# Kernel optimization log

Hardware: AMD Instinct MI355X
Metric: run time of the kernel (lower is better)

## Reference

```python
import jax, jax.numpy as jnp
import numpy as np

N, C, H, E = 4096, 512, 8, 131072
D = C // H
ALPHA = 0.5
EPS = 1e-5


def layer_norm(x, g, b):
    mu = jnp.mean(x, axis=-1, keepdims=True)
    var = jnp.mean((x - mu) ** 2, axis=-1, keepdims=True)
    return (x - mu) * jax.lax.rsqrt(var + EPS) * g + b


def setup_inputs() -> dict:
    key = jax.random.key(0)
    ks = jax.random.split(key, 20)
    s = 0.02
    return {
        "x": jax.random.normal(ks[0], (N, C), jnp.float32),
        "edge_index": jax.random.randint(ks[1], (2, E), 0, N, jnp.int32),
        "local_w": jax.random.normal(ks[2], (C, C), jnp.float32) * s,
        "local_b": jnp.zeros((C,), jnp.float32),
        "in_proj_w": jax.random.normal(ks[3], (3 * C, C), jnp.float32) * s,
        "in_proj_b": jnp.zeros((3 * C,), jnp.float32),
        "attn_out_w": jax.random.normal(ks[4], (C, C), jnp.float32) * s,
        "attn_out_b": jnp.zeros((C,), jnp.float32),
        "output_w": jax.random.normal(ks[5], (C, C), jnp.float32) * s,
        "output_b": jnp.zeros((C,), jnp.float32),
        "norm1_g": jnp.ones((C,), jnp.float32),
        "norm1_b": jnp.zeros((C,), jnp.float32),
        "norm2_g": jnp.ones((C,), jnp.float32),
        "norm2_b": jnp.zeros((C,), jnp.float32),
        "ffn_w1": jax.random.normal(ks[6], (2 * C, C), jnp.float32) * s,
        "ffn_b1": jnp.zeros((2 * C,), jnp.float32),
        "ffn_w2": jax.random.normal(ks[7], (C, 2 * C), jnp.float32) * s,
        "ffn_b2": jnp.zeros((C,), jnp.float32),
    }


def reference(x, edge_index, local_w, local_b, in_proj_w, in_proj_b,
              attn_out_w, attn_out_b, output_w, output_b,
              norm1_g, norm1_b, norm2_g, norm2_b,
              ffn_w1, ffn_b1, ffn_w2, ffn_b2):
    src, dst = edge_index[0], edge_index[1]

    # local branch: linear then scatter-mean over incoming edges
    local_h = x @ local_w.T + local_b                       # [N,C]
    summed = jax.ops.segment_sum(local_h[src], dst, num_segments=N)
    cnt = jax.ops.segment_sum(jnp.ones((E,), x.dtype), dst, num_segments=N)
    local_out = summed / jnp.maximum(cnt, 1.0)[:, None]

    # global branch: full self-attention over all nodes
    qkv = x @ in_proj_w.T + in_proj_b                       # [N,3C]
    q, k, v = jnp.split(qkv, 3, axis=-1)
    q = q.reshape(N, H, D)
    k = k.reshape(N, H, D)
    v = v.reshape(N, H, D)
    scores = jnp.einsum('nhd,mhd->hnm', q, k) / jnp.sqrt(jnp.asarray(D, x.dtype))
    attn = jax.nn.softmax(scores, axis=-1)                  # [H,N,N]
    ctx = jnp.einsum('hnm,mhd->nhd', attn, v).reshape(N, C)
    global_out = ctx @ attn_out_w.T + attn_out_b

    mixed = ALPHA * local_out + (1.0 - ALPHA) * global_out
    hidden = layer_norm(x + (mixed @ output_w.T + output_b), norm1_g, norm1_b)

    ff = jax.nn.gelu(hidden @ ffn_w1.T + ffn_b1, approximate=False) @ ffn_w2.T + ffn_b2
    return layer_norm(hidden + ff, norm2_g, norm2_b)
```

## Files before the change

kernel.cpp:

```cpp
#include <hip/hip_runtime.h>


#define N_NODES 4096
#define C_DIM   512
#define H_HEADS 8
#define D_HEAD  64
#define E_EDGES 131072

typedef unsigned short u16;
typedef unsigned int   u32;
typedef u16   u16x8  __attribute__((ext_vector_type(8)));
typedef __bf16 bf16x8 __attribute__((ext_vector_type(8)));
typedef float  f32x4  __attribute__((ext_vector_type(4)));
typedef u32    u32x4  __attribute__((ext_vector_type(4)));

__device__ __forceinline__ float b2f(u16 u) {
  unsigned int i = ((unsigned int)u) << 16;
  return __builtin_bit_cast(float, i);
}
__device__ __forceinline__ u16 f2b(float f) {
  unsigned int i = __builtin_bit_cast(unsigned int, f);
  i += 0x7fffu + ((i >> 16) & 1u);
  return (u16)(i >> 16);
}
__device__ __forceinline__ u32 cvtpk(float lo, float hi) {
  u32 r;
  asm("v_cvt_pk_bf16_f32 %0, %1, %2" : "=v"(r) : "v"(lo), "v"(hi));
  return r;
}
__device__ __forceinline__ void pl32swap(u32& x, u32& y) {
  asm("v_permlane32_swap_b32 %0, %1" : "+v"(x), "+v"(y));
}
__device__ __forceinline__ void pl16swap(u32& x, u32& y) {
  asm("v_permlane16_swap_b32 %0, %1" : "+v"(x), "+v"(y));
}
__device__ __forceinline__ void glds16(const u16* g, u16* l) {
  __builtin_amdgcn_global_load_lds(
      (const __attribute__((address_space(1))) void*)g,
      (__attribute__((address_space(3))) void*)l, 16, 0, 0);
}

struct CvtArgs {
  const float* src[7];
  u16* dst[7];
  int n[7];
  int* deg;
};

__global__ __launch_bounds__(256) void cvt_multi(CvtArgs a) {
  const int t = blockIdx.y;
  if (t == 7) {
    const int i = blockIdx.x * 256 + threadIdx.x;
    if (i < N_NODES) a.deg[i] = 0;
    return;
  }
  const int i = (blockIdx.x * 256 + threadIdx.x) * 8;
  if (i >= a.n[t]) return;
  const float* s = a.src[t] + i;
  f32x4 v0 = *(const f32x4*)s;
  f32x4 v1 = *(const f32x4*)(s + 4);
  u16x8 o;
  o[0]=f2b(v0[0]); o[1]=f2b(v0[1]); o[2]=f2b(v0[2]); o[3]=f2b(v0[3]);
  o[4]=f2b(v1[0]); o[5]=f2b(v1[1]); o[6]=f2b(v1[2]); o[7]=f2b(v1[3]);
  *(u16x8*)(a.dst[t] + i) = o;
}

template<int EPI>
__global__ __launch_bounds__(256) void gemm_bt(
    const u16* __restrict__ A, const u16* __restrict__ W,
    const float* __restrict__ bias, void* __restrict__ outp,
    int M, int Nout, int K,
    const float* __restrict__ mloc)
{
  const int tid  = threadIdx.x;
  const int lane = tid & 63, wave = tid >> 6;
  const int quad = lane >> 4, l16 = lane & 15;
  const int wm = wave >> 1, wn = wave & 1;
  const int bm = blockIdx.x, bnb = blockIdx.y;

  __shared__ __align__(16) u16 As[64][128];
  __shared__ __align__(16) u16 Ws[64][128];

  f32x4 acc[2][2] = {};

  const int lr4 = lane >> 4, gs = lane & 15;
  const int g8e = (gs ^ lr4) * 8;
  const int g8o = (gs ^ (4 + lr4)) * 8;
  const u16* aw[8];
#pragma unroll
  for (int c = 0; c < 4; ++c) {
    const int g8 = (c & 1) ? g8o : g8e;
    aw[c]     = A + (size_t)(bm  * 64 + wave * 16 + c * 4 + lr4) * K + g8;
    aw[4 + c] = W + (size_t)(bnb * 64 + wave * 16 + c * 4 + lr4) * K + g8;
  }

  for (int k0 = 0; k0 < K; k0 += 128) {
    __syncthreads();
#pragma unroll
    for (int c = 0; c < 4; ++c) {
      glds16(aw[c] + k0,     &As[wave * 16 + c * 4][0]);
      glds16(aw[4 + c] + k0, &Ws[wave * 16 + c * 4][0]);
    }
    __syncthreads();
#pragma unroll
    for (int ks = 0; ks < 4; ++ks) {
      const int slot = ((ks * 4 + quad) ^ (l16 & 7)) * 8;
      bf16x8 af[2], bf[2];
      af[0] = *(const bf16x8*)&As[wm * 32 +      l16][slot];
      af[1] = *(const bf16x8*)&As[wm * 32 + 16 + l16][slot];
      bf[0] = *(const bf16x8*)&Ws[wn * 32 +      l16][slot];
      bf[1] = *(const bf16x8*)&Ws[wn * 32 + 16 + l16][slot];
#pragma unroll
      for (int i = 0; i < 2; ++i)
#pragma unroll
        for (int j = 0; j < 2; ++j)
          acc[i][j] = __builtin_amdgcn_mfma_f32_16x16x32_bf16(af[i], bf[j], acc[i][j], 0, 0, 0);
    }
  }

#pragma unroll
  for (int i = 0; i < 2; ++i)
#pragma unroll
    for (int j = 0; j < 2; ++j) {
      const int col = bnb * 64 + wn * 32 + j * 16 + l16;
      const float bias_v = bias[col];
#pragma unroll
      for (int r = 0; r < 4; ++r) {
        const int row = bm * 64 + wm * 32 + i * 16 + quad * 4 + r;
        float v = acc[i][j][r] + bias_v;
        const size_t o = (size_t)row * Nout + col;
        if constexpr (EPI == 1) {
          ((float*)outp)[o] = v;
        } else if constexpr (EPI == 2) {
          float gl = 0.5f * v * (1.0f + erff(v * 0.70710678118654752f));
          ((u16*)outp)[o] = f2b(gl);
        } else {
          ((u16*)outp)[o] = f2b(0.5f * mloc[o] + 0.5f * v);
        }
      }
    }
}

__global__ __launch_bounds__(256) void gemm128(
    const u16* __restrict__ A, const u16* __restrict__ W,
    const float* __restrict__ bias0, const float* __restrict__ bias1,
    u16* __restrict__ out0, u16* __restrict__ out1,
    int M, int Nout, int K,
    const int* __restrict__ ei, int* __restrict__ deg)
{
  const int tid  = threadIdx.x;
  if (blockIdx.y == 16) {
#pragma unroll
    for (int i = 0; i < 16; ++i) {
      const int e = blockIdx.x * 4096 + i * 256 + tid;
      atomicAdd(&deg[ei[E_EDGES + e]], 1);
    }
    return;
  }
  const int lane = tid & 63, wave = tid >> 6;
  const int quad = lane >> 4, l16 = lane & 15;
  const int wm = wave >> 1, wn = wave & 1;
  const int bm = blockIdx.x, bnb = blockIdx.y;

  __shared__ __align__(16) u16 As[128][64];
  __shared__ __align__(16) u16 Ws[128][64];

  f32x4 acc[4][4] = {};

  const int lr = lane >> 3, gs = lane & 7;
  const int g8 = (gs ^ lr) * 8;
  const u16* ab = A + (size_t)(bm  * 128 + wave * 32 + lr) * K + g8;
  const u16* wb = W + (size_t)(bnb * 128 + wave * 32 + lr) * K + g8;

  for (int k0 = 0; k0 < K; k0 += 64) {
    __syncthreads();
#pragma unroll
    for (int c = 0; c < 4; ++c) {
      glds16(ab + (size_t)(c * 8) * K + k0, &As[wave * 32 + c * 8][0]);
      glds16(wb + (size_t)(c * 8) * K + k0, &Ws[wave * 32 + c * 8][0]);
    }
    __syncthreads();
#pragma unroll
    for (int ks = 0; ks < 2; ++ks) {
      const int slot = ((ks * 4 + quad) ^ (l16 & 7)) * 8;
      bf16x8 af[4], bf[4];
#pragma unroll
      for (int am = 0; am < 4; ++am)
        af[am] = *(const bf16x8*)&As[wm * 64 + am * 16 + l16][slot];
#pragma unroll
      for (int bn = 0; bn < 4; ++bn)
        bf[bn] = *(const bf16x8*)&Ws[wn * 64 + bn * 16 + l16][slot];
#pragma unroll
      for (int am = 0; am < 4; ++am)
#pragma unroll
        for (int bn = 0; bn < 4; ++bn)
          acc[am][bn] = __builtin_amdgcn_mfma_f32_16x16x32_bf16(af[am], bf[bn], acc[am][bn], 0, 0, 0);
    }
  }

#pragma unroll
  for (int am = 0; am < 4; ++am)
#pragma unroll
    for (int bn = 0; bn < 4; ++bn) {
      const int col = bnb * 128 + wn * 64 + bn * 16 + l16;
      const float bias_v = (col < 512) ? bias0[col] : bias1[col - 512];
#pragma unroll
      for (int r = 0; r < 4; ++r) {
        const int row = bm * 128 + wm * 64 + am * 16 + quad * 4 + r;
        float v = acc[am][bn][r] + bias_v;
        if (col < 512) out0[(size_t)row * 512 + col] = f2b(v);
        else           out1[(size_t)row * 1536 + (col - 512)] = f2b(v);
      }
    }
}

__global__ __launch_bounds__(256) void scan_vtrans(
    const int* __restrict__ deg, int* __restrict__ off, int* __restrict__ cursor,
    const u16* __restrict__ qkv, u16* __restrict__ vt)
{
  if (blockIdx.x == 512) {
    __shared__ int part[256];
    const int t = threadIdx.x;
    int v[16];
    int s = 0;
#pragma unroll
    for (int i = 0; i < 16; ++i) { v[i] = deg[t * 16 + i]; s += v[i]; }
    part[t] = s;
    __syncthreads();
    for (int d = 1; d < 256; d <<= 1) {
      int val = (t >= d) ? part[t - d] : 0;
      __syncthreads();
      if (t >= d) part[t] += val;
      __syncthreads();
    }
    int prefix = (t == 0) ? 0 : part[t - 1];
#pragma unroll
    for (int i = 0; i < 16; ++i) {
      off[t * 16 + i] = prefix;
      cursor[t * 16 + i] = prefix;
      prefix += v[i];
    }
    if (t == 255) off[4096] = prefix;
    return;
  }
  const int tid = threadIdx.x;
  const int d = tid & 63, mg = tid >> 6;
  const int h = blockIdx.x >> 6, mt = blockIdx.x & 63;
  const int m0 = mt * 64 + mg * 16;
  u16 buf[16];
#pragma unroll
  for (int i = 0; i < 16; ++i)
    buf[i] = qkv[(size_t)(m0 + i) * 1536 + 1024 + h * 64 + d];
  u16x8 w0, w1;
#pragma unroll
  for (int i = 0; i < 8; ++i) { w0[i] = buf[i]; w1[i] = buf[8 + i]; }
  u16* op = vt + (size_t)(h * 64 + d) * N_NODES + m0;
  *(u16x8*)op = w0;
  *(u16x8*)(op + 8) = w1;
}

template<int SPLITS>
__global__ __launch_bounds__(256) void attn_kernel(
    const u16* __restrict__ qkv, const u16* __restrict__ vt,
    u16* __restrict__ opart, float* __restrict__ lpart,
    const int* __restrict__ ei, int* __restrict__ cursor, int* __restrict__ csr)
{
  const int tid = threadIdx.x, wave = tid >> 6, lane = tid & 63;
  const int split = blockIdx.z;
  if (split == SPLITS) {
    const int sblk = blockIdx.y * 32 + blockIdx.x;
#pragma unroll
    for (int i = 0; i < 2; ++i) {
      const int e = sblk * 512 + i * 256 + tid;
      const int s = ei[e];
      const int d = ei[E_EDGES + e];
      const int p = atomicAdd(&cursor[d], 1);
      csr[p] = s;
    }
    return;
  }
  const int quad = lane >> 4, l16 = lane & 15;
  const int h = blockIdx.y, tile = blockIdx.x;

  __shared__ __align__(16) u16 Ks[2][64][64];
  __shared__ __align__(16) u16 Vts[2][64][64];

  const float QSCALE = 0.18033688011112042f;
  bf16x8 aq[2][2];
#pragma unroll
  for (int mb = 0; mb < 2; ++mb) {
    const int qrow = tile * 128 + wave * 32 + mb * 16 + l16;
    const u16* qp = qkv + (size_t)qrow * 1536 + h * 64 + quad * 8;
    u16x8 q0 = *(const u16x8*)qp;
    u16x8 q1 = *(const u16x8*)(qp + 32);
    u16x8 s0, s1;
#pragma unroll
    for (int i = 0; i < 8; ++i) {
      s0[i] = f2b(b2f(q0[i]) * QSCALE);
      s1[i] = f2b(b2f(q1[i]) * QSCALE);
    }
    aq[mb][0] = __builtin_bit_cast(bf16x8, s0);
    aq[mb][1] = __builtin_bit_cast(bf16x8, s1);
  }

  f32x4 O[2][4] = {};
  float lsum[2] = {};

  const int lr = lane >> 3, gs = lane & 7;
  const int g8 = (gs ^ lr) * 8;
  const int R0 = wave * 16 + lr;

  const u16* kp = qkv + (size_t)R0 * 1536 + 512 + h * 64 + g8;
  const u16* vp = vt + (size_t)(h * 64 + R0) * N_NODES + g8;

  const int mt0 = split * (64 / SPLITS), mt1 = (split + 1) * (64 / SPLITS);

  {
    const size_t ko = (size_t)mt0 * 64 * 1536;
    glds16(kp + ko,            &Ks[0][wave * 16][0]);
    glds16(kp + ko + 8 * 1536, &Ks[0][wave * 16 + 8][0]);
    glds16(vp + mt0 * 64,                        &Vts[0][wave * 16][0]);
    glds16(vp + mt0 * 64 + 8 * N_NODES,          &Vts[0][wave * 16 + 8][0]);
  }

  for (int mt = mt0; mt < mt1; ++mt) {
    const int cur = (mt - mt0) & 1;
    if (mt + 1 < mt1) {
      const size_t ko = (size_t)(mt + 1) * 64 * 1536;
      glds16(kp + ko,            &Ks[cur ^ 1][wave * 16][0]);
      glds16(kp + ko + 8 * 1536, &Ks[cur ^ 1][wave * 16 + 8][0]);
      glds16(vp + (mt + 1) * 64,                 &Vts[cur ^ 1][wave * 16][0]);
      glds16(vp + (mt + 1) * 64 + 8 * N_NODES,   &Vts[cur ^ 1][wave * 16 + 8][0]);
      asm volatile("s_waitcnt vmcnt(4)" ::: "memory");
    } else {
      asm volatile("s_waitcnt vmcnt(0)" ::: "memory");
    }
    __builtin_amdgcn_s_barrier();
    __builtin_amdgcn_sched_barrier(0);

    f32x4 st[2][4] = {};
    __builtin_amdgcn_s_setprio(1);
#pragma unroll
    for (int ks = 0; ks < 2; ++ks) {
      const int slot = ((ks * 4 + quad) ^ (l16 & 7)) * 8;
      bf16x8 af[4];
#pragma unroll
      for (int jn = 0; jn < 4; ++jn)
        af[jn] = *(const bf16x8*)&Ks[cur][jn * 16 + l16][slot];
#pragma unroll
      for (int mb = 0; mb < 2; ++mb)
#pragma unroll
        for (int jn = 0; jn < 4; ++jn)
          st[mb][jn] = __builtin_amdgcn_mfma_f32_16x16x32_bf16(af[jn], aq[mb][ks], st[mb][jn], 0, 0, 0);
    }
    __builtin_amdgcn_s_setprio(0);

    bf16x8 pa[2][2];
#pragma unroll
    for (int mb = 0; mb < 2; ++mb) {
      u32 pk[4][2];
#pragma unroll
      for (int jn = 0; jn < 4; ++jn) {
        float p0 = __builtin_amdgcn_exp2f(st[mb][jn][0]);
        float p1 = __builtin_amdgcn_exp2f(st[mb][jn][1]);
        float p2 = __builtin_amdgcn_exp2f(st[mb][jn][2]);
        float p3 = __builtin_amdgcn_exp2f(st[mb][jn][3]);
        lsum[mb] += (p0 + p1) + (p2 + p3);
        pk[jn][0] = cvtpk(p0, p1);
        pk[jn][1] = cvtpk(p2, p3);
      }
#pragma unroll
      for (int ks = 0; ks < 2; ++ks) {
        u32 x0 = pk[2 * ks][0], y0 = pk[2 * ks + 1][0];
        u32 x1 = pk[2 * ks][1], y1 = pk[2 * ks + 1][1];
        pl32swap(x0, y0); pl16swap(x0, y0);
        pl32swap(x1, y1); pl16swap(x1, y1);
        u32x4 av;
        av[0] = x0; av[1] = x1; av[2] = y0; av[3] = y1;
        pa[mb][ks] = __builtin_bit_cast(bf16x8, av);
      }
    }

    __builtin_amdgcn_s_setprio(1);
#pragma unroll
    for (int ks = 0; ks < 2; ++ks) {
      const int slot = ((ks * 4 + quad) ^ (l16 & 7)) * 8;
      bf16x8 bv[4];
#pragma unroll
      for (int jd = 0; jd < 4; ++jd)
        bv[jd] = *(const bf16x8*)&Vts[cur][jd * 16 + l16][slot];
#pragma unroll
      for (int mb = 0; mb < 2; ++mb)
#pragma unroll
        for (int jd = 0; jd < 4; ++jd)
          O[mb][jd] = __builtin_amdgcn_mfma_f32_16x16x32_bf16(pa[mb][ks], bv[jd], O[mb][jd], 0, 0, 0);
    }
    __builtin_amdgcn_s_setprio(0);
    __builtin_amdgcn_s_barrier();
  }

#pragma unroll
  for (int mb = 0; mb < 2; ++mb) {
    float ls = lsum[mb];
    ls += __shfl_xor(ls, 16);
    ls += __shfl_xor(ls, 32);
#pragma unroll
    for (int r = 0; r < 4; ++r) {
      const int row = tile * 128 + wave * 32 + mb * 16 + quad * 4 + r;
      u16* orow = opart + ((size_t)split * N_NODES + row) * C_DIM + h * 64;
#pragma unroll
      for (int jd = 0; jd < 4; ++jd)
        orow[jd * 16 + l16] = f2b(O[mb][jd][r]);
    }
    if (lane < 16) {
      const int row = tile * 128 + wave * 32 + mb * 16 + l16;
      lpart[((size_t)split * N_NODES + row) * H_HEADS + h] = ls;
    }
  }
}

template<int SPLITS>
__global__ __launch_bounds__(256) void combine_gather(
    const u16* __restrict__ opart, const float* __restrict__ lpart,
    u16* __restrict__ ctx,
    const int* __restrict__ off, const int* __restrict__ csr,
    const u16* __restrict__ lh, float* __restrict__ lo)
{
  if (blockIdx.y == 0) {
    const int wave = threadIdx.x >> 6, lane = threadIdx.x & 63;
    const int n = blockIdx.x * 4 + wave;
    const int j0 = off[n], j1 = off[n + 1];
    float acc[8] = {};
    for (int j = j0; j < j1; ++j) {
      const int s = csr[j];
      const u16x8 v = *(const u16x8*)(lh + (size_t)s * C_DIM + lane * 8);
#pragma unroll
      for (int i = 0; i < 8; ++i) acc[i] += b2f(v[i]);
    }
    const float inv = 1.0f / fmaxf((float)(j1 - j0), 1.0f);
    f32x4 o0, o1;
#pragma unroll
    for (int i = 0; i < 4; ++i) { o0[i] = acc[i] * inv; o1[i] = acc[4 + i] * inv; }
    float* op = lo + (size_t)n * C_DIM + lane * 8;
    *(f32x4*)op = o0;
    *(f32x4*)(op + 4) = o1;
    return;
  }
  const size_t base = (size_t)(blockIdx.x * 256 + threadIdx.x) * 8;
  const int row = (int)(base >> 9);
  const int h = (int)((base & 511) >> 6);
  float l = 0.0f;
#pragma unroll
  for (int s = 0; s < SPLITS; ++s)
    l += lpart[(size_t)s * N_NODES * H_HEADS + (size_t)row * H_HEADS + h];
  const float inv = 1.0f / l;
  float o[8] = {};
#pragma unroll
  for (int s = 0; s < SPLITS; ++s) {
    const u16x8 p = *(const u16x8*)(opart + (size_t)s * N_NODES * C_DIM + base);
#pragma unroll
    for (int i = 0; i < 8; ++i) o[i] += b2f(p[i]);
  }
  u16x8 ob;
#pragma unroll
  for (int i = 0; i < 8; ++i) ob[i] = f2b(o[i] * inv);
  *(u16x8*)(ctx + base) = ob;
}

__global__ __launch_bounds__(256) void ln1_kernel(
    const float* __restrict__ x, const float* __restrict__ pr,
    const float* __restrict__ g, const float* __restrict__ b,
    u16* __restrict__ hb, float* __restrict__ hf)
{
  const int wave = threadIdx.x >> 6, lane = threadIdx.x & 63;
  const int row = blockIdx.x * 4 + wave;
  const int c0 = lane * 8;
  const size_t base = (size_t)row * C_DIM + c0;
  f32x4 x0 = *(const f32x4*)(x + base);
  f32x4 x1 = *(const f32x4*)(x + base + 4);
  f32x4 p0 = *(const f32x4*)(pr + base);
  f32x4 p1 = *(const f32x4*)(pr + base + 4);
  float v[8];
#pragma unroll
  for (int i = 0; i < 4; ++i) { v[i] = x0[i] + p0[i]; v[4 + i] = x1[i] + p1[i]; }
  float sum = 0, sq = 0;
#pragma unroll
  for (int i = 0; i < 8; ++i) { sum += v[i]; sq += v[i] * v[i]; }
  for (int off = 1; off < 64; off <<= 1) { sum += __shfl_xor(sum, off); sq += __shfl_xor(sq, off); }
  const float mean = sum * (1.0f / C_DIM);
  const float var  = sq * (1.0f / C_DIM) - mean * mean;
  const float rstd = rsqrtf(var + 1e-5f);
  f32x4 g0 = *(const f32x4*)(g + c0), g1 = *(const f32x4*)(g + c0 + 4);
  f32x4 b0 = *(const f32x4*)(b + c0), b1 = *(const f32x4*)(b + c0 + 4);
  u16x8 ob; f32x4 h0, h1;
#pragma unroll
  for (int i = 0; i < 4; ++i) {
    float hv0 = (v[i]     - mean) * rstd * g0[i] + b0[i];
    float hv1 = (v[4 + i] - mean) * rstd * g1[i] + b1[i];
    h0[i] = hv0; h1[i] = hv1;
    ob[i] = f2b(hv0); ob[4 + i] = f2b(hv1);
  }
  *(u16x8*)(hb + base) = ob;
  *(f32x4*)(hf + base) = h0;
  *(f32x4*)(hf + base + 4) = h1;
}

__global__ __launch_bounds__(256) void ln2_kernel(
    const float* __restrict__ a, const float* __restrict__ c,
    const float* __restrict__ g, const float* __restrict__ b,
    float* __restrict__ out)
{
  const int wave = threadIdx.x >> 6, lane = threadIdx.x & 63;
  const int row = blockIdx.x * 4 + wave;
  const int c0 = lane * 8;
  const size_t base = (size_t)row * C_DIM + c0;
  f32x4 a0 = *(const f32x4*)(a + base), a1 = *(const f32x4*)(a + base + 4);
  f32x4 c0v = *(const f32x4*)(c + base), c1v = *(const f32x4*)(c + base + 4);
  float v[8];
#pragma unroll
  for (int i = 0; i < 4; ++i) { v[i] = a0[i] + c0v[i]; v[4 + i] = a1[i] + c1v[i]; }
  float sum = 0, sq = 0;
#pragma unroll
  for (int i = 0; i < 8; ++i) { sum += v[i]; sq += v[i] * v[i]; }
  for (int off = 1; off < 64; off <<= 1) { sum += __shfl_xor(sum, off); sq += __shfl_xor(sq, off); }
  const float mean = sum * (1.0f / C_DIM);
  const float var  = sq * (1.0f / C_DIM) - mean * mean;
  const float rstd = rsqrtf(var + 1e-5f);
  f32x4 g0 = *(const f32x4*)(g + c0), g1 = *(const f32x4*)(g + c0 + 4);
  f32x4 b0 = *(const f32x4*)(b + c0), b1 = *(const f32x4*)(b + c0 + 4);
  f32x4 h0, h1;
#pragma unroll
  for (int i = 0; i < 4; ++i) {
    h0[i] = (v[i]     - mean) * rstd * g0[i] + b0[i];
    h1[i] = (v[4 + i] - mean) * rstd * g1[i] + b1[i];
  }
  *(f32x4*)(out + base) = h0;
  *(f32x4*)(out + base + 4) = h1;
}

extern "C" void kernel_launch(void* const* d_in, const int* in_sizes, int n_in,
                              void* d_out, int out_size, void* d_ws, size_t ws_size,
                              hipStream_t stream) {
  const float* x          = (const float*)d_in[0];
  const int*   ei         = (const int*)d_in[1];
  const float* local_w    = (const float*)d_in[2];
  const float* local_b    = (const float*)d_in[3];
  const float* in_proj_w  = (const float*)d_in[4];
  const float* in_proj_b  = (const float*)d_in[5];
  const float* attn_out_w = (const float*)d_in[6];
  const float* attn_out_b = (const float*)d_in[7];
  const float* output_w   = (const float*)d_in[8];
  const float* output_b   = (const float*)d_in[9];
  const float* n1g = (const float*)d_in[10];
  const float* n1b = (const float*)d_in[11];
  const float* n2g = (const float*)d_in[12];
  const float* n2b = (const float*)d_in[13];
  const float* ffn_w1 = (const float*)d_in[14];
  const float* ffn_b1 = (const float*)d_in[15];
  const float* ffn_w2 = (const float*)d_in[16];
  const float* ffn_b2 = (const float*)d_in[17];
  float* out = (float*)d_out;

  char* ws = (char*)d_ws;
  size_t o = 0;
  float* local_out = (float*)(ws + o); o += (size_t)N_NODES * C_DIM * 4;
  int* deg    = (int*)(ws + o); o += (N_NODES) * 4;
  int* off    = (int*)(ws + o); o += (N_NODES + 16) * 4;
  int* cursor = (int*)(ws + o); o += (N_NODES) * 4;
  int* csr    = (int*)(ws + o); o += (size_t)E_EDGES * 4;
  u16* xb   = (u16*)(ws + o); o += (size_t)N_NODES * C_DIM * 2;
  u16* wbLQ = (u16*)(ws + o); o += (size_t)4 * C_DIM * C_DIM * 2;
  u16* wbA  = (u16*)(ws + o); o += (size_t)C_DIM * C_DIM * 2;
  u16* wbO  = (u16*)(ws + o); o += (size_t)C_DIM * C_DIM * 2;
  u16* wbF1 = (u16*)(ws + o); o += (size_t)2 * C_DIM * C_DIM * 2;
  u16* wbF2 = (u16*)(ws + o); o += (size_t)2 * C_DIM * C_DIM * 2;
  u16* local_h   = (u16*)(ws + o); o += (size_t)N_NODES * C_DIM * 2;
  u16* qkvb      = (u16*)(ws + o); o += (size_t)N_NODES * 3 * C_DIM * 2;
  u16* ctxb      = (u16*)(ws + o); o += (size_t)N_NODES * C_DIM * 2;
  u16* mixed     = (u16*)(ws + o); o += (size_t)N_NODES * C_DIM * 2;
  u16* hidden_bf = (u16*)(ws + o); o += (size_t)N_NODES * C_DIM * 2;
  float* hidden_f = (float*)(ws + o); o += (size_t)N_NODES * C_DIM * 4;
  u16* ff1       = (u16*)(ws + o); o += (size_t)N_NODES * 2 * C_DIM * 2;
  float* proj  = (float*)qkvb;
  float* ff2   = (float*)local_out;
  u16*   vt    = xb;
  u16* opart4 = (u16*)(ws + o);
  float* lpart4 = (float*)(ws + o + (size_t)4 * N_NODES * C_DIM * 2);
  const size_t need4 = o + (size_t)4 * N_NODES * C_DIM * 2 + (size_t)4 * N_NODES * H_HEADS * 4;
  const bool use4 = (ws_size >= need4);
  u16* opart2 = (u16*)hidden_bf;
  float* lpart2 = (float*)(opart2 + (size_t)2 * N_NODES * C_DIM);

  CvtArgs ca;
  ca.src[0] = x;          ca.dst[0] = xb;   ca.n[0] = N_NODES * C_DIM;
  ca.src[1] = local_w;    ca.dst[1] = wbLQ;                  ca.n[1] = C_DIM * C_DIM;
  ca.src[2] = in_proj_w;  ca.dst[2] = wbLQ + C_DIM * C_DIM;  ca.n[2] = 3 * C_DIM * C_DIM;
  ca.src[3] = attn_out_w; ca.dst[3] = wbA;  ca.n[3] = C_DIM * C_DIM;
  ca.src[4] = output_w;   ca.dst[4] = wbO;  ca.n[4] = C_DIM * C_DIM;
  ca.src[5] = ffn_w1;     ca.dst[5] = wbF1; ca.n[5] = 2 * C_DIM * C_DIM;
  ca.src[6] = ffn_w2;     ca.dst[6] = wbF2; ca.n[6] = 2 * C_DIM * C_DIM;
  ca.deg = deg;
  cvt_multi<<<dim3(N_NODES * C_DIM / 2048, 8), 256, 0, stream>>>(ca);

  gemm128<<<dim3(32, 17), 256, 0, stream>>>(xb, wbLQ, local_b, in_proj_b,
      local_h, qkvb, N_NODES, 4 * C_DIM, C_DIM, ei, deg);

  scan_vtrans<<<513, 256, 0, stream>>>(deg, off, cursor, qkvb, vt);

  if (use4) {
    attn_kernel<4><<<dim3(32, 8, 5), 256, 0, stream>>>(qkvb, vt, opart4, lpart4,
        ei, cursor, csr);
    combine_gather<4><<<dim3(1024, 2), 256, 0, stream>>>(opart4, lpart4, ctxb,
        off, csr, local_h, local_out);
  } else {
    attn_kernel<2><<<dim3(32, 8, 3), 256, 0, stream>>>(qkvb, vt, opart2, lpart2,
        ei, cursor, csr);
    combine_gather<2><<<dim3(1024, 2), 256, 0, stream>>>(opart2, lpart2, ctxb,
        off, csr, local_h, local_out);
  }

  gemm_bt<3><<<dim3(64, 8), 256, 0, stream>>>(ctxb, wbA, attn_out_b, mixed,
      N_NODES, C_DIM, C_DIM, local_out);

  gemm_bt<1><<<dim3(64, 8), 256, 0, stream>>>(mixed, wbO, output_b, proj,
      N_NODES, C_DIM, C_DIM, nullptr);
  ln1_kernel<<<N_NODES / 4, 256, 0, stream>>>(x, proj, n1g, n1b, hidden_bf, hidden_f);

  gemm_bt<2><<<dim3(64, 16), 256, 0, stream>>>(hidden_bf, wbF1, ffn_b1, ff1,
      N_NODES, 2 * C_DIM, C_DIM, nullptr);
  gemm_bt<1><<<dim3(64, 8), 256, 0, stream>>>(ff1, wbF2, ffn_b2, ff2,
      N_NODES, C_DIM, 2 * C_DIM, nullptr);
  ln2_kernel<<<N_NODES / 4, 256, 0, stream>>>(hidden_f, ff2, n2g, n2b, out);
}
```

Baseline: 255.2 us.

## Software-pipeline PV MFMA behind next QK, LDS-transpose V, unroll gather loop

The attention loop now issues the previous tile's P·V MFMAs right after the current tile's QK^T MFMAs, using a triple-buffered V tile so the exp/convert of one tile can overlap matrix work of another. The V transpose kernel stages a 64x64 block through swizzled shared memory, giving coalesced vector loads and stores instead of strided scalar loads. The CSR gather-mean loop is unrolled by four so four independent row loads are in flight at once. These changes cost extra LDS for the third V buffer and more registers for the carried P fragments, which could lower occupancy.

```diff
diff --git a/kernel.cpp b/kernel.cpp
--- a/kernel.cpp
+++ b/kernel.cpp
@@ -243,20 +243,29 @@
     if (t == 255) off[4096] = prefix;
     return;
   }
+  __shared__ __align__(16) u16 T[64][64];
   const int tid = threadIdx.x;
-  const int d = tid & 63, mg = tid >> 6;
   const int h = blockIdx.x >> 6, mt = blockIdx.x & 63;
-  const int m0 = mt * 64 + mg * 16;
-  u16 buf[16];
-#pragma unroll
-  for (int i = 0; i < 16; ++i)
-    buf[i] = qkv[(size_t)(m0 + i) * 1536 + 1024 + h * 64 + d];
-  u16x8 w0, w1;
-#pragma unroll
-  for (int i = 0; i < 8; ++i) { w0[i] = buf[i]; w1[i] = buf[8 + i]; }
-  u16* op = vt + (size_t)(h * 64 + d) * N_NODES + m0;
-  *(u16x8*)op = w0;
-  *(u16x8*)(op + 8) = w1;
+  const int m0 = mt * 64;
+  const int c  = tid & 7;
+  const int mr = tid >> 3;
+#pragma unroll
+  for (int half = 0; half < 2; ++half) {
+    const int m = mr + half * 32;
+    const u16x8 v = *(const u16x8*)(qkv + (size_t)(m0 + m) * 1536 + 1024 + h * 64 + c * 8);
+    *(u16x8*)&T[m][((c ^ (m >> 3)) * 8)] = v;
+  }
+  __syncthreads();
+#pragma unroll
+  for (int half = 0; half < 2; ++half) {
+    const int q = tid + half * 256;
+    const int d = q >> 3, mc = q & 7;
+    u16x8 w;
+#pragma unroll
+    for (int e = 0; e < 8; ++e)
+      w[e] = T[mc * 8 + e][(((d >> 3) ^ mc) * 8) + (d & 7)];
+    *(u16x8*)(vt + (size_t)(h * 64 + d) * N_NODES + m0 + mc * 8) = w;
+  }
 }
 
 template<int SPLITS>
@@ -283,7 +292,7 @@
   const int h = blockIdx.y, tile = blockIdx.x;
 
   __shared__ __align__(16) u16 Ks[2][64][64];
-  __shared__ __align__(16) u16 Vts[2][64][64];
+  __shared__ __align__(16) u16 Vts[3][64][64];
 
   const float QSCALE = 0.18033688011112042f;
   bf16x8 aq[2][2];
@@ -319,18 +328,21 @@
     const size_t ko = (size_t)mt0 * 64 * 1536;
     glds16(kp + ko,            &Ks[0][wave * 16][0]);
     glds16(kp + ko + 8 * 1536, &Ks[0][wave * 16 + 8][0]);
-    glds16(vp + mt0 * 64,                        &Vts[0][wave * 16][0]);
-    glds16(vp + mt0 * 64 + 8 * N_NODES,          &Vts[0][wave * 16 + 8][0]);
-  }
+    glds16(vp + mt0 * 64,               &Vts[0][wave * 16][0]);
+    glds16(vp + mt0 * 64 + 8 * N_NODES, &Vts[0][wave * 16 + 8][0]);
+  }
+
+  bf16x8 paP[2][2];
+  int vprev = 2, vcur = 0, vnext = 1;
 
   for (int mt = mt0; mt < mt1; ++mt) {
-    const int cur = (mt - mt0) & 1;
+    const int kc = (mt - mt0) & 1;
     if (mt + 1 < mt1) {
       const size_t ko = (size_t)(mt + 1) * 64 * 1536;
-      glds16(kp + ko,            &Ks[cur ^ 1][wave * 16][0]);
-      glds16(kp + ko + 8 * 1536, &Ks[cur ^ 1][wave * 16 + 8][0]);
-      glds16(vp + (mt + 1) * 64,                 &Vts[cur ^ 1][wave * 16][0]);
-      glds16(vp + (mt + 1) * 64 + 8 * N_NODES,   &Vts[cur ^ 1][wave * 16 + 8][0]);
+      glds16(kp + ko,            &Ks[kc ^ 1][wave * 16][0]);
+      glds16(kp + ko + 8 * 1536, &Ks[kc ^ 1][wave * 16 + 8][0]);
+      glds16(vp + (mt + 1) * 64,               &Vts[vnext][wave * 16][0]);
+      glds16(vp + (mt + 1) * 64 + 8 * N_NODES, &Vts[vnext][wave * 16 + 8][0]);
       asm volatile("s_waitcnt vmcnt(4)" ::: "memory");
     } else {
       asm volatile("s_waitcnt vmcnt(0)" ::: "memory");
@@ -338,24 +350,38 @@
     __builtin_amdgcn_s_barrier();
     __builtin_amdgcn_sched_barrier(0);
 
+    __builtin_amdgcn_s_setprio(1);
     f32x4 st[2][4] = {};
-    __builtin_amdgcn_s_setprio(1);
 #pragma unroll
     for (int ks = 0; ks < 2; ++ks) {
       const int slot = ((ks * 4 + quad) ^ (l16 & 7)) * 8;
       bf16x8 af[4];
 #pragma unroll
       for (int jn = 0; jn < 4; ++jn)
-        af[jn] = *(const bf16x8*)&Ks[cur][jn * 16 + l16][slot];
+        af[jn] = *(const bf16x8*)&Ks[kc][jn * 16 + l16][slot];
 #pragma unroll
       for (int mb = 0; mb < 2; ++mb)
 #pragma unroll
         for (int jn = 0; jn < 4; ++jn)
           st[mb][jn] = __builtin_amdgcn_mfma_f32_16x16x32_bf16(af[jn], aq[mb][ks], st[mb][jn], 0, 0, 0);
     }
+    if (mt > mt0) {
+#pragma unroll
+      for (int ks = 0; ks < 2; ++ks) {
+        const int slot = ((ks * 4 + quad) ^ (l16 & 7)) * 8;
+        bf16x8 bv[4];
+#pragma unroll
+        for (int jd = 0; jd < 4; ++jd)
+          bv[jd] = *(const bf16x8*)&Vts[vprev][jd * 16 + l16][slot];
+#pragma unroll
+        for (int mb = 0; mb < 2; ++mb)
+#pragma unroll
+          for (int jd = 0; jd < 4; ++jd)
+            O[mb][jd] = __builtin_amdgcn_mfma_f32_16x16x32_bf16(paP[mb][ks], bv[jd], O[mb][jd], 0, 0, 0);
+      }
+    }
     __builtin_amdgcn_s_setprio(0);
 
-    bf16x8 pa[2][2];
 #pragma unroll
     for (int mb = 0; mb < 2; ++mb) {
       u32 pk[4][2];
@@ -377,26 +403,26 @@
         pl32swap(x1, y1); pl16swap(x1, y1);
         u32x4 av;
         av[0] = x0; av[1] = x1; av[2] = y0; av[3] = y1;
-        pa[mb][ks] = __builtin_bit_cast(bf16x8, av);
+        paP[mb][ks] = __builtin_bit_cast(bf16x8, av);
       }
     }
 
-    __builtin_amdgcn_s_setprio(1);
-#pragma unroll
-    for (int ks = 0; ks < 2; ++ks) {
-      const int slot = ((ks * 4 + quad) ^ (l16 & 7)) * 8;
-      bf16x8 bv[4];
+    __builtin_amdgcn_s_barrier();
+    const int vr = vprev; vprev = vcur; vcur = vnext; vnext = vr;
+  }
+
+#pragma unroll
+  for (int ks = 0; ks < 2; ++ks) {
+    const int slot = ((ks * 4 + quad) ^ (l16 & 7)) * 8;
+    bf16x8 bv[4];
+#pragma unroll
+    for (int jd = 0; jd < 4; ++jd)
+      bv[jd] = *(const bf16x8*)&Vts[vprev][jd * 16 + l16][slot];
+#pragma unroll
+    for (int mb = 0; mb < 2; ++mb)
 #pragma unroll
       for (int jd = 0; jd < 4; ++jd)
-        bv[jd] = *(const bf16x8*)&Vts[cur][jd * 16 + l16][slot];
-#pragma unroll
-      for (int mb = 0; mb < 2; ++mb)
-#pragma unroll
-        for (int jd = 0; jd < 4; ++jd)
-          O[mb][jd] = __builtin_amdgcn_mfma_f32_16x16x32_bf16(pa[mb][ks], bv[jd], O[mb][jd], 0, 0, 0);
-    }
-    __builtin_amdgcn_s_setprio(0);
-    __builtin_amdgcn_s_barrier();
+        O[mb][jd] = __builtin_amdgcn_mfma_f32_16x16x32_bf16(paP[mb][ks], bv[jd], O[mb][jd], 0, 0, 0);
   }
 
 #pragma unroll
@@ -431,7 +457,18 @@
     const int n = blockIdx.x * 4 + wave;
     const int j0 = off[n], j1 = off[n + 1];
     float acc[8] = {};
-    for (int j = j0; j < j1; ++j) {
+    int j = j0;
+    for (; j + 4 <= j1; j += 4) {
+      const int s0 = csr[j], s1 = csr[j + 1], s2 = csr[j + 2], s3 = csr[j + 3];
+      const u16x8 v0 = *(const u16x8*)(lh + (size_t)s0 * C_DIM + lane * 8);
+      const u16x8 v1 = *(const u16x8*)(lh + (size_t)s1 * C_DIM + lane * 8);
+      const u16x8 v2 = *(const u16x8*)(lh + (size_t)s2 * C_DIM + lane * 8);
+      const u16x8 v3 = *(const u16x8*)(lh + (size_t)s3 * C_DIM + lane * 8);
+#pragma unroll
+      for (int i = 0; i < 8; ++i)
+        acc[i] += (b2f(v0[i]) + b2f(v1[i])) + (b2f(v2[i]) + b2f(v3[i]));
+    }
+    for (; j < j1; ++j) {
       const int s = csr[j];
       const u16x8 v = *(const u16x8*)(lh + (size_t)s * C_DIM + lane * 8);
 #pragma unroll
```

Result: no change. 252.1 us (-1.2%).
